# Kernel tuning notes

Measured on AMD Instinct MI355X. Metric: run time of the kernel, lower is better.

Reference implementation:

```python
import jax, jax.numpy as jnp
import numpy as np

DIM = 1024
HEADS = 16
HEAD_DIM = DIM // HEADS
MLP_HIDDEN = int(DIM * 0.7)  # 716
EPS = 1e-5


def _ln(x, g, b):
    m = jnp.mean(x, axis=-1, keepdims=True)
    v = jnp.mean(jnp.square(x - m), axis=-1, keepdims=True)
    return (x - m) * jax.lax.rsqrt(v + EPS) * g + b


def setup_inputs() -> dict:
    key = jax.random.key(0)
    ks = jax.random.split(key, 8)
    B, N = 4, 1024
    x = jax.random.normal(ks[0], (B, N, DIM), dtype=jnp.float32)
    s = 0.02
    return {
        "x": x,
        "norm_g": jnp.ones((DIM,), jnp.float32),
        "norm_b": jnp.zeros((DIM,), jnp.float32),
        "W1": jax.random.normal(ks[1], (DIM, 3 * DIM + MLP_HIDDEN), jnp.float32) * s,
        "b1": jnp.zeros((3 * DIM + MLP_HIDDEN,), jnp.float32),
        "qn_g": jnp.ones((HEAD_DIM,), jnp.float32),
        "qn_b": jnp.zeros((HEAD_DIM,), jnp.float32),
        "kn_g": jnp.ones((HEAD_DIM,), jnp.float32),
        "kn_b": jnp.zeros((HEAD_DIM,), jnp.float32),
        "projW": jax.random.normal(ks[2], (DIM, DIM), jnp.float32) * s,
        "projb": jnp.zeros((DIM,), jnp.float32),
        "mlpW": jax.random.normal(ks[3], (MLP_HIDDEN, DIM), jnp.float32) * s,  # mlp_bias=False
        "W2": jax.random.normal(ks[4], (2 * DIM, DIM), jnp.float32) * s,
        "b2": jnp.zeros((DIM,), jnp.float32),
        "ls_g": jnp.full((DIM,), 1e-5, jnp.float32),
    }


def reference(x, norm_g, norm_b, W1, b1, qn_g, qn_b, kn_g, kn_b,
              projW, projb, mlpW, W2, b2, ls_g):
    B, N, C = x.shape
    norm_x = _ln(x, norm_g, norm_b)
    f1 = norm_x @ W1 + b1  # (B, N, 3*dim + mlp_hidden)
    qkv, mlp_hidden = f1[..., :3 * DIM], f1[..., 3 * DIM:]
    # (B, N, 3, H, hd) -> (3, B, H, N, hd)
    qkv = qkv.reshape(B, N, 3, HEADS, HEAD_DIM).transpose(2, 0, 3, 1, 4)
    q, k, v = qkv[0], qkv[1], qkv[2]
    q = _ln(q, qn_g, qn_b)
    k = _ln(k, kn_g, kn_b)
    attn = jnp.einsum('bhnd,bhmd->bhnm', q, k) * (HEAD_DIM ** -0.5)
    attn = jax.nn.softmax(attn, axis=-1)
    xo = jnp.einsum('bhnm,bhmd->bhnd', attn, v)
    xo = xo.transpose(0, 2, 1, 3).reshape(B, N, DIM)
    attn_out = xo @ projW + projb
    mlp_out = jax.nn.gelu(mlp_hidden, approximate=False) @ mlpW  # no bias
    combined = jnp.concatenate([attn_out, mlp_out], axis=-1)
    out = x + (combined @ W2 + b2) * ls_g
    return out
```

## Files before the change

### kernel.cpp

```cpp
#include <hip/hip_runtime.h>
#include <cstdint>
#include <cstddef>

typedef unsigned short u16;
typedef unsigned char u8;
typedef __attribute__((ext_vector_type(8))) u16 u16x8;
typedef __attribute__((ext_vector_type(8))) __bf16 bf16x8;
typedef __attribute__((ext_vector_type(4))) float f32x4;
typedef __attribute__((ext_vector_type(16))) float f32x16;
typedef __attribute__((ext_vector_type(4))) int i32x4;
typedef __attribute__((ext_vector_type(8))) int i32x8;
typedef __attribute__((ext_vector_type(2))) int i32x2;

__device__ __forceinline__ u16 f2bf(float f) {
  unsigned u = __builtin_bit_cast(unsigned, f);
  return (u16)((u + 0x7FFFu + ((u >> 16) & 1u)) >> 16);
}
__device__ __forceinline__ float bf2f(u16 h) {
  return __builtin_bit_cast(float, (unsigned)h << 16);
}
__device__ __forceinline__ u8 f2fp8(float f) {
  return (u8)(__builtin_amdgcn_cvt_pk_fp8_f32(f, 0.f, 0, false) & 0xFF);
}
__device__ __forceinline__ f32x16 mfma32(u16x8 a, u16x8 b, f32x16 c) {
  return __builtin_amdgcn_mfma_f32_32x32x16_bf16(
      __builtin_bit_cast(bf16x8, a), __builtin_bit_cast(bf16x8, b), c, 0, 0, 0);
}
__device__ __forceinline__ unsigned cvtpk_bf16(float lo, float hi) {
  unsigned r;
  asm("v_cvt_pk_bf16_f32 %0, %1, %2" : "=v"(r) : "v"(lo), "v"(hi));
  return r;
}
__device__ __forceinline__ float exp2_fast(float x) {
  float r;
  asm("v_exp_f32 %0, %1" : "=v"(r) : "v"(x));
  return r;
}
__device__ __forceinline__ void plswap(unsigned& a, unsigned& b) {
  i32x2 r = __builtin_amdgcn_permlane32_swap((int)a, (int)b, false, false);
  a = (unsigned)r[0];
  b = (unsigned)r[1];
}
__device__ __forceinline__ void load_lds16(const void* g, void* l) {
  __builtin_amdgcn_global_load_lds(
      (const __attribute__((address_space(1))) void*)g,
      (__attribute__((address_space(3))) void*)l, 16, 0, 0);
}

__global__ __launch_bounds__(256) void k_pre(
    const float* __restrict__ W1, const float* __restrict__ projW,
    const float* __restrict__ mlpW, const float* __restrict__ W2,
    u8* __restrict__ W1t, u8* __restrict__ pWt, u8* __restrict__ mWt,
    u8* __restrict__ W2t, const float* __restrict__ x,
    const float* __restrict__ g, const float* __restrict__ b,
    u8* __restrict__ nx8) {
  __shared__ float t[32][33];
  __shared__ float red[8];
  const int L = blockIdx.x;
  const int tid = threadIdx.x;
  if (L < 7680) {
    const float* src;
    u8* dst;
    int R, C, dR, dC, bx, by;
    if (L < 3840) {
      src = W1; dst = W1t; R = 1024; C = 3788; dR = 1024; dC = 3840;
      bx = L % 120; by = L / 120;
    } else if (L < 4864) {
      int tq = L - 3840;
      src = projW; dst = pWt; R = 1024; C = 1024; dR = 1024; dC = 1024;
      bx = tq & 31; by = tq >> 5;
    } else if (L < 5632) {
      int tq = L - 4864;
      src = mlpW; dst = mWt; R = 716; C = 1024; dR = 768; dC = 1024;
      bx = tq & 31; by = tq >> 5;
    } else {
      int tq = L - 5632;
      src = W2; dst = W2t; R = 2048; C = 1024; dR = 2048; dC = 1024;
      bx = tq & 31; by = tq >> 5;
    }
    const int n0 = bx * 32, k0 = by * 32;
    const int tx = tid & 31, ty = tid >> 5;
#pragma unroll
    for (int j = 0; j < 4; ++j) {
      int kk = k0 + ty + 8 * j, nn = n0 + tx;
      float v = (kk < R && nn < C) ? src[(size_t)kk * C + nn] : 0.f;
      t[ty + 8 * j][tx] = v;
    }
    __syncthreads();
#pragma unroll
    for (int j = 0; j < 4; ++j) {
      int nn = n0 + ty + 8 * j, kk = k0 + tx;
      if (nn < dC && kk < dR) dst[(size_t)nn * dR + kk] = f2fp8(t[tx][ty + 8 * j]);
    }
  } else {
    const int row = L - 7680;
    float4 v = ((const float4*)(x + (size_t)row * 1024))[tid];
    float s = v.x + v.y + v.z + v.w;
    float ss = v.x * v.x + v.y * v.y + v.z * v.z + v.w * v.w;
#pragma unroll
    for (int off = 1; off < 64; off <<= 1) {
      s += __shfl_xor(s, off);
      ss += __shfl_xor(ss, off);
    }
    const int wid = tid >> 6, lane = tid & 63;
    if (lane == 0) { red[wid] = s; red[4 + wid] = ss; }
    __syncthreads();
    s = red[0] + red[1] + red[2] + red[3];
    ss = red[4] + red[5] + red[6] + red[7];
    const float mean = s * (1.f / 1024.f);
    const float var = ss * (1.f / 1024.f) - mean * mean;
    const float rstd = rsqrtf(var + 1e-5f);
    float4 gv = ((const float4*)g)[tid];
    float4 bv = ((const float4*)b)[tid];
    float y0 = (v.x - mean) * rstd * gv.x + bv.x;
    float y1 = (v.y - mean) * rstd * gv.y + bv.y;
    float y2 = (v.z - mean) * rstd * gv.z + bv.z;
    float y3 = (v.w - mean) * rstd * gv.w + bv.w;
    int pk = __builtin_amdgcn_cvt_pk_fp8_f32(y0, y1, 0, false);
    pk = __builtin_amdgcn_cvt_pk_fp8_f32(y2, y3, pk, true);
    ((int*)(nx8 + (size_t)row * 1024))[tid] = pk;
  }
}

__device__ __forceinline__ void gemm_fp8_core(const u8* __restrict__ A,
                                              const u8* __restrict__ B, int K,
                                              u8* Alds, u8* Blds,
                                              f32x16 (&acc)[2][2], int tid) {
  const int lane = tid & 63, wave = tid >> 6;
  const int h = lane >> 5, r32 = lane & 31;
  const int wrow = (wave >> 1) * 64, wcol = (wave & 1) * 64;
  const int srow0 = tid >> 2, spos = tid & 3;
  const int nk = K >> 6;
  auto STAGE = [&](int t, int bb) {
#pragma unroll
    for (int p = 0; p < 2; ++p) {
      const int row = p * 64 + srow0;
      const int c = spos ^ ((row >> 1) & 3);
      const size_t go = (size_t)row * K + (size_t)t * 64 + c * 16;
      load_lds16(A + go, Alds + bb * 8192 + (p * 256 + tid) * 16);
      load_lds16(B + go, Blds + bb * 8192 + (p * 256 + tid) * 16);
    }
  };
  STAGE(0, 0);
  STAGE(1, 1);
  asm volatile("s_waitcnt vmcnt(4)" ::: "memory");
  __builtin_amdgcn_s_barrier();
  int cur = 0;
  for (int kt = 0; kt < nk; ++kt) {
    const u8* Ac = Alds + cur * 8192;
    const u8* Bc = Blds + cur * 8192;
    i32x8 af[2], bf[2];
#pragma unroll
    for (int t = 0; t < 2; ++t) {
      {
        const int row = wrow + t * 32 + r32;
        const int sw = (row >> 1) & 3;
        i32x4 lo = *(const i32x4*)(Ac + row * 64 + ((2 * h) ^ sw) * 16);
        i32x4 hi = *(const i32x4*)(Ac + row * 64 + ((2 * h + 1) ^ sw) * 16);
        i32x8 a;
        a[0] = lo[0]; a[1] = lo[1]; a[2] = lo[2]; a[3] = lo[3];
        a[4] = hi[0]; a[5] = hi[1]; a[6] = hi[2]; a[7] = hi[3];
        af[t] = a;
      }
      {
        const int row = wcol + t * 32 + r32;
        const int sw = (row >> 1) & 3;
        i32x4 lo = *(const i32x4*)(Bc + row * 64 + ((2 * h) ^ sw) * 16);
        i32x4 hi = *(const i32x4*)(Bc + row * 64 + ((2 * h + 1) ^ sw) * 16);
        i32x8 b8;
        b8[0] = lo[0]; b8[1] = lo[1]; b8[2] = lo[2]; b8[3] = lo[3];
        b8[4] = hi[0]; b8[5] = hi[1]; b8[6] = hi[2]; b8[7] = hi[3];
        bf[t] = b8;
      }
    }
    if (kt + 2 < nk) STAGE(kt + 2, cur == 0 ? 2 : cur - 1);
#pragma unroll
    for (int i = 0; i < 2; ++i)
#pragma unroll
      for (int j = 0; j < 2; ++j)
        acc[i][j] = __builtin_amdgcn_mfma_scale_f32_32x32x64_f8f6f4(
            af[i], bf[j], acc[i][j], 0, 0, 0, 0x7F7F7F7F, 0, 0x7F7F7F7F);
    if (kt + 1 < nk) {
      if (kt + 2 < nk)
        asm volatile("s_waitcnt vmcnt(4)" ::: "memory");
      else
        asm volatile("s_waitcnt vmcnt(0)" ::: "memory");
      __builtin_amdgcn_s_barrier();
    }
    cur = (cur == 2) ? 0 : cur + 1;
  }
}

__device__ __forceinline__ void gemm_fp8_core64(const u8* __restrict__ A,
                                                const u8* __restrict__ B, int K,
                                                u8* Alds, u8* Blds,
                                                f32x16 (&acc)[2], int tid) {
  const int lane = tid & 63, wave = tid >> 6;
  const int h = lane >> 5, r32 = lane & 31;
  const int wrow = (wave >> 1) * 32, wcol = (wave & 1) * 64;
  const int nk = K >> 6;
  const int ra = tid >> 2, posa = tid & 3;
  const int ca = posa ^ ((ra >> 1) & 3);
  auto STAGE = [&](int t, int bb) {
    const size_t k0 = (size_t)t * 64;
    load_lds16(A + (size_t)ra * K + k0 + ca * 16, Alds + bb * 4096 + tid * 16);
#pragma unroll
    for (int p = 0; p < 2; ++p) {
      const int s = tid + 256 * p;
      const int r = s >> 2, pos = s & 3;
      const int c = pos ^ ((r >> 1) & 3);
      load_lds16(B + (size_t)r * K + k0 + c * 16, Blds + bb * 8192 + s * 16);
    }
  };
  STAGE(0, 0);
  STAGE(1, 1);
  asm volatile("s_waitcnt vmcnt(3)" ::: "memory");
  __builtin_amdgcn_s_barrier();
  int cur = 0;
  for (int kt = 0; kt < nk; ++kt) {
    const u8* Ac = Alds + cur * 4096;
    const u8* Bc = Blds + cur * 8192;
    i32x8 af, bf[2];
    {
      const int row = wrow + r32;
      const int sw = (row >> 1) & 3;
      i32x4 lo = *(const i32x4*)(Ac + row * 64 + ((2 * h) ^ sw) * 16);
      i32x4 hi = *(const i32x4*)(Ac + row * 64 + ((2 * h + 1) ^ sw) * 16);
      af[0] = lo[0]; af[1] = lo[1]; af[2] = lo[2]; af[3] = lo[3];
      af[4] = hi[0]; af[5] = hi[1]; af[6] = hi[2]; af[7] = hi[3];
    }
#pragma unroll
    for (int t = 0; t < 2; ++t) {
      const int row = wcol + t * 32 + r32;
      const int sw = (row >> 1) & 3;
      i32x4 lo = *(const i32x4*)(Bc + row * 64 + ((2 * h) ^ sw) * 16);
      i32x4 hi = *(const i32x4*)(Bc + row * 64 + ((2 * h + 1) ^ sw) * 16);
      i32x8 b8;
      b8[0] = lo[0]; b8[1] = lo[1]; b8[2] = lo[2]; b8[3] = lo[3];
      b8[4] = hi[0]; b8[5] = hi[1]; b8[6] = hi[2]; b8[7] = hi[3];
      bf[t] = b8;
    }
    if (kt + 2 < nk) STAGE(kt + 2, cur == 0 ? 2 : cur - 1);
#pragma unroll
    for (int j = 0; j < 2; ++j)
      acc[j] = __builtin_amdgcn_mfma_scale_f32_32x32x64_f8f6f4(
          af, bf[j], acc[j], 0, 0, 0, 0x7F7F7F7F, 0, 0x7F7F7F7F);
    if (kt + 1 < nk) {
      if (kt + 2 < nk)
        asm volatile("s_waitcnt vmcnt(3)" ::: "memory");
      else
        asm volatile("s_waitcnt vmcnt(0)" ::: "memory");
      __builtin_amdgcn_s_barrier();
    }
    cur = (cur == 2) ? 0 : cur + 1;
  }
}

__global__ __launch_bounds__(256) void k_gemm1(const u8* __restrict__ nx8,
                                               const u8* __restrict__ W1t,
                                               u16* __restrict__ f1,
                                               const float* __restrict__ b1) {
  __shared__ __align__(16) u8 Alds[3 * 128 * 64];
  __shared__ __align__(16) u8 Blds[3 * 128 * 64];
  const int tid = threadIdx.x, bm = blockIdx.y, bn = blockIdx.x;
  f32x16 acc[2][2];
#pragma unroll
  for (int i = 0; i < 2; ++i)
#pragma unroll
    for (int j = 0; j < 2; ++j)
#pragma unroll
      for (int r = 0; r < 16; ++r) acc[i][j][r] = 0.f;
  gemm_fp8_core(nx8 + (size_t)bm * 128 * 1024, W1t + (size_t)bn * 128 * 1024, 1024,
                Alds, Blds, acc, tid);
  const int lane = tid & 63, wave = tid >> 6;
  const int h = lane >> 5, r32 = lane & 31;
  const int wrow = (wave >> 1) * 64, wcol = (wave & 1) * 64;
#pragma unroll
  for (int i = 0; i < 2; ++i)
#pragma unroll
    for (int j = 0; j < 2; ++j) {
      const int col = bn * 128 + wcol + j * 32 + r32;
      const float bs = (col < 3788) ? b1[col] : 0.f;
#pragma unroll
      for (int r = 0; r < 16; ++r) {
        const int row = bm * 128 + wrow + i * 32 + 4 * h + (r & 3) + 8 * (r >> 2);
        f1[(size_t)row * 3840 + col] = f2bf(acc[i][j][r] + bs);
      }
    }
}

__global__ __launch_bounds__(256) void k_gemm_pm(
    const u8* __restrict__ xo, const u8* __restrict__ pWt,
    const u8* __restrict__ gel, const u8* __restrict__ mWt,
    u8* __restrict__ comb, const float* __restrict__ projb) {
  __shared__ __align__(16) u8 Alds[3 * 64 * 64];
  __shared__ __align__(16) u8 Blds[3 * 128 * 64];
  const int tid = threadIdx.x, bm = blockIdx.y, bnq = blockIdx.x;
  const u8* A;
  const u8* B;
  int K, colbase;
  const float* bias;
  if (bnq < 8) {
    A = xo + (size_t)bm * 64 * 1024;
    B = pWt + (size_t)bnq * 128 * 1024;
    K = 1024; colbase = bnq * 128; bias = projb;
  } else {
    A = gel + (size_t)bm * 64 * 768;
    B = mWt + (size_t)(bnq - 8) * 128 * 768;
    K = 768; colbase = 1024 + (bnq - 8) * 128; bias = nullptr;
  }
  f32x16 acc[2];
#pragma unroll
  for (int j = 0; j < 2; ++j)
#pragma unroll
    for (int r = 0; r < 16; ++r) acc[j][r] = 0.f;
  gemm_fp8_core64(A, B, K, Alds, Blds, acc, tid);
  const int lane = tid & 63, wave = tid >> 6;
  const int h = lane >> 5, r32 = lane & 31;
  const int wrow = (wave >> 1) * 32, wcol = (wave & 1) * 64;
#pragma unroll
  for (int j = 0; j < 2; ++j) {
    const int col = colbase + wcol + j * 32 + r32;
    const float bs = (bias != nullptr) ? bias[col] : 0.f;
#pragma unroll
    for (int r = 0; r < 16; ++r) {
      const int row = bm * 64 + wrow + 4 * h + (r & 3) + 8 * (r >> 2);
      comb[(size_t)row * 2048 + col] = f2fp8(acc[j][r] + bs);
    }
  }
}

__global__ __launch_bounds__(256) void k_gemm_fin(const u8* __restrict__ comb,
                                                  const u8* __restrict__ W2t,
                                                  float* __restrict__ out,
                                                  const float* __restrict__ b2,
                                                  const float* __restrict__ x,
                                                  const float* __restrict__ lsg) {
  __shared__ __align__(16) u8 Alds[3 * 64 * 64];
  __shared__ __align__(16) u8 Blds[3 * 128 * 64];
  const int tid = threadIdx.x, bm = blockIdx.y, bn = blockIdx.x;
  f32x16 acc[2];
#pragma unroll
  for (int j = 0; j < 2; ++j)
#pragma unroll
    for (int r = 0; r < 16; ++r) acc[j][r] = 0.f;
  gemm_fp8_core64(comb + (size_t)bm * 64 * 2048, W2t + (size_t)bn * 128 * 2048, 2048,
                  Alds, Blds, acc, tid);
  const int lane = tid & 63, wave = tid >> 6;
  const int h = lane >> 5, r32 = lane & 31;
  const int wrow = (wave >> 1) * 32, wcol = (wave & 1) * 64;
#pragma unroll
  for (int j = 0; j < 2; ++j) {
    const int col = bn * 128 + wcol + j * 32 + r32;
    const float bs = b2[col], ls = lsg[col];
#pragma unroll
    for (int r = 0; r < 16; ++r) {
      const int row = bm * 64 + wrow + 4 * h + (r & 3) + 8 * (r >> 2);
      out[(size_t)row * 1024 + col] =
          x[(size_t)row * 1024 + col] + (acc[j][r] + bs) * ls;
    }
  }
}

__global__ __launch_bounds__(256) void k_mid(const u16* __restrict__ f1,
                                             const float* __restrict__ qg,
                                             const float* __restrict__ qbb,
                                             const float* __restrict__ kg,
                                             const float* __restrict__ kbb,
                                             u16* __restrict__ q,
                                             u16* __restrict__ k,
                                             u8* __restrict__ gel,
                                             u16* __restrict__ vtb) {
  __shared__ u16 tt[32][33];
  const int tid = threadIdx.x;
  const int L = blockIdx.x;
  if (L < 4096) {
    const int row = L;
    const int rem = tid >> 3;
    const int which = rem >> 4, h = rem & 15;
    const int e8 = (tid & 7) * 8;
    u16x8 xv = *(const u16x8*)(f1 + (size_t)row * 3840 + which * 1024 + h * 64 + e8);
    float xf[8];
    float s1 = 0.f, s2 = 0.f;
#pragma unroll
    for (int e = 0; e < 8; ++e) {
      xf[e] = bf2f(xv[e]);
      s1 += xf[e];
      s2 += xf[e] * xf[e];
    }
#pragma unroll
    for (int off = 1; off < 8; off <<= 1) {
      s1 += __shfl_xor(s1, off);
      s2 += __shfl_xor(s2, off);
    }
    const float mean = s1 * (1.f / 64.f);
    const float var = s2 * (1.f / 64.f) - mean * mean;
    const float rstd = rsqrtf(var + 1e-5f);
    const float* g = (which == 0) ? qg : kg;
    const float* bb = (which == 0) ? qbb : kbb;
    float4 g0 = ((const float4*)g)[e8 >> 2], g1 = ((const float4*)g)[(e8 >> 2) + 1];
    float4 b0 = ((const float4*)bb)[e8 >> 2], b1 = ((const float4*)bb)[(e8 >> 2) + 1];
    float gv[8] = {g0.x, g0.y, g0.z, g0.w, g1.x, g1.y, g1.z, g1.w};
    float bv[8] = {b0.x, b0.y, b0.z, b0.w, b1.x, b1.y, b1.z, b1.w};
    u16x8 o;
#pragma unroll
    for (int e = 0; e < 8; ++e) o[e] = f2bf((xf[e] - mean) * rstd * gv[e] + bv[e]);
    const int b = row >> 10, n = row & 1023;
    u16* dst = (which == 0) ? q : k;
    *(u16x8*)(dst + ((size_t)(b * 16 + h) * 1024 + n) * 64 + e8) = o;
  } else if (L < 5632) {
    const int id = (L - 4096) * 256 + tid;
    const int row = id / 96, c8 = id - row * 96;
    u16x8 xv = *(const u16x8*)(f1 + (size_t)row * 3840 + 3072 + c8 * 8);
    float rr[8];
#pragma unroll
    for (int e = 0; e < 8; ++e) {
      const int col = c8 * 8 + e;
      rr[e] = 0.f;
      if (col < 716) {
        float xx = bf2f(xv[e]);
        rr[e] = 0.5f * xx * (1.f + erff(xx * 0.70710678118654752f));
      }
    }
    int p0 = __builtin_amdgcn_cvt_pk_fp8_f32(rr[0], rr[1], 0, false);
    p0 = __builtin_amdgcn_cvt_pk_fp8_f32(rr[2], rr[3], p0, true);
    int p1 = __builtin_amdgcn_cvt_pk_fp8_f32(rr[4], rr[5], 0, false);
    p1 = __builtin_amdgcn_cvt_pk_fp8_f32(rr[6], rr[7], p1, true);
    uint2 pk;
    pk.x = (unsigned)p0;
    pk.y = (unsigned)p1;
    *(uint2*)(gel + (size_t)row * 768 + c8 * 8) = pk;
  } else {
    const int t = L - 5632;
    const int xq = t & 1, yq = (t >> 1) & 31, z = t >> 6;
    const int b = z >> 4, h = z & 15;
    const int d0 = xq * 32, n0 = yq * 32;
    const int tx = tid & 31, ty = tid >> 5;
#pragma unroll
    for (int j = 0; j < 4; ++j)
      tt[ty + 8 * j][tx] =
          f1[(size_t)(b * 1024 + n0 + ty + 8 * j) * 3840 + 2048 + h * 64 + d0 + tx];
    __syncthreads();
#pragma unroll
    for (int j = 0; j < 4; ++j)
      vtb[(size_t)z * 65536 + (size_t)(d0 + ty + 8 * j) * 1024 + n0 + tx] =
          tt[tx][ty + 8 * j];
  }
}

__global__ __launch_bounds__(64) void k_flash(const u16* __restrict__ q,
                                              const u16* __restrict__ k,
                                              const u16* __restrict__ vt,
                                              u8* __restrict__ xo) {
  __shared__ __align__(16) u16 Kl[2][32 * 64];
  __shared__ __align__(16) u16 Vl[2][64 * 32];
  const int lane = threadIdx.x & 63;
  const int l31 = lane & 31, h = lane >> 5;
  const int L = blockIdx.x;
  const int xcd = L & 7, i = L >> 3;
  const int bh = xcd * 8 + (i & 7);
  const int qt = i >> 3;
  const int qrow0 = qt * 32;
  const u16* qb = q + ((size_t)bh * 1024 + qrow0) * 64;
  const u16* kb = k + (size_t)bh * 1024 * 64;
  const u16* vb = vt + (size_t)bh * 64 * 1024;

  u16x8 qf[4];
#pragma unroll
  for (int ds = 0; ds < 4; ++ds)
    qf[ds] = *(const u16x8*)(qb + (size_t)l31 * 64 + ds * 16 + h * 8);
  asm volatile("s_waitcnt vmcnt(0)" ::: "memory");

  f32x16 O[2];
#pragma unroll
  for (int d2 = 0; d2 < 2; ++d2)
#pragma unroll
    for (int r = 0; r < 16; ++r) O[d2][r] = 0.f;
  float lacc = 0.f;

  auto STAGE = [&](int t, int bb) {
#pragma unroll
    for (int p = 0; p < 4; ++p) {
      const int s = lane + 64 * p;
      const int kr = s >> 3, kslot = s & 7;
      const int kc = kslot ^ ((kr ^ (kr >> 3)) & 7);
      load_lds16(kb + (size_t)(t * 32 + kr) * 64 + kc * 8, (u16*)Kl[bb] + s * 8);
      const int vr = s >> 2, vslot = s & 3;
      const int vc = vslot ^ ((vr >> 1) & 3);
      load_lds16(vb + (size_t)vr * 1024 + t * 32 + vc * 8, (u16*)Vl[bb] + s * 8);
    }
  };
  STAGE(0, 0);
  STAGE(1, 1);

  const int swzk = (l31 & 7) ^ ((l31 >> 3) & 3);
  for (int t = 0; t < 32; ++t) {
    if (t < 31)
      asm volatile("s_waitcnt vmcnt(8)" ::: "memory");
    else
      asm volatile("s_waitcnt vmcnt(0)" ::: "memory");
    const u16* Kc = (const u16*)Kl[t & 1];
    const u16* Vc = (const u16*)Vl[t & 1];
    u16x8 kf[4], vf[4];
#pragma unroll
    for (int ds = 0; ds < 4; ++ds) {
      const int pos = (ds * 2 + h) ^ swzk;
      kf[ds] = *(const u16x8*)(Kc + l31 * 64 + pos * 8);
    }
#pragma unroll
    for (int m = 0; m < 2; ++m)
#pragma unroll
      for (int d2 = 0; d2 < 2; ++d2) {
        const int vr = d2 * 32 + l31;
        const int pos = (m * 2 + h) ^ ((vr >> 1) & 3);
        vf[m * 2 + d2] = *(const u16x8*)(Vc + vr * 32 + pos * 8);
      }
    asm volatile("s_waitcnt lgkmcnt(0)" ::: "memory");
    if (t + 2 < 32) STAGE(t + 2, t & 1);

    f32x16 S;
#pragma unroll
    for (int r = 0; r < 16; ++r) S[r] = 0.f;
    __builtin_amdgcn_s_setprio(1);
#pragma unroll
    for (int ds = 0; ds < 4; ++ds) S = mfma32(kf[ds], qf[ds], S);
    __builtin_amdgcn_s_setprio(0);

#pragma unroll
    for (int r = 0; r < 16; ++r) {
      float pv = exp2_fast(S[r] * 0.18033688011112042f);
      S[r] = pv;
      lacc += pv;
    }

    __builtin_amdgcn_s_setprio(1);
#pragma unroll
    for (int m = 0; m < 2; ++m) {
      const int ro = m * 8;
      unsigned w0 = cvtpk_bf16(S[ro + 0], S[ro + 1]);
      unsigned w2 = cvtpk_bf16(S[ro + 4], S[ro + 5]);
      unsigned w1 = cvtpk_bf16(S[ro + 2], S[ro + 3]);
      unsigned w3 = cvtpk_bf16(S[ro + 6], S[ro + 7]);
      plswap(w0, w2);
      plswap(w1, w3);
      i32x4 aw;
      aw[0] = (int)w0; aw[1] = (int)w1; aw[2] = (int)w2; aw[3] = (int)w3;
      const u16x8 pa = __builtin_bit_cast(u16x8, aw);
#pragma unroll
      for (int d2 = 0; d2 < 2; ++d2) O[d2] = mfma32(pa, vf[m * 2 + d2], O[d2]);
    }
    __builtin_amdgcn_s_setprio(0);
  }

  lacc += __shfl_xor(lacc, 32);
  const float inv = 1.f / lacc;
  const int b = bh >> 4, hh = bh & 15;
#pragma unroll
  for (int r = 0; r < 16; ++r) {
    const int qr = (r & 3) + 8 * (r >> 2) + 4 * h;
    const float invr = __shfl(inv, qr);
    u8* orow = xo + (size_t)(b * 1024 + qrow0 + qr) * 1024 + hh * 64;
    orow[l31] = f2fp8(O[0][r] * invr);
    orow[32 + l31] = f2fp8(O[1][r] * invr);
  }
}

extern "C" void kernel_launch(void* const* d_in, const int* in_sizes, int n_in,
                              void* d_out, int out_size, void* d_ws, size_t ws_size,
                              hipStream_t stream) {
  (void)in_sizes; (void)n_in; (void)out_size; (void)ws_size;
  const float* x      = (const float*)d_in[0];
  const float* norm_g = (const float*)d_in[1];
  const float* norm_b = (const float*)d_in[2];
  const float* W1     = (const float*)d_in[3];
  const float* b1     = (const float*)d_in[4];
  const float* qn_g   = (const float*)d_in[5];
  const float* qn_b   = (const float*)d_in[6];
  const float* kn_g   = (const float*)d_in[7];
  const float* kn_b   = (const float*)d_in[8];
  const float* projW  = (const float*)d_in[9];
  const float* projb  = (const float*)d_in[10];
  const float* mlpW   = (const float*)d_in[11];
  const float* W2     = (const float*)d_in[12];
  const float* b2     = (const float*)d_in[13];
  const float* ls_g   = (const float*)d_in[14];

  char* ws = (char*)d_ws;
  u8*  W1t8 = (u8*)(ws + 0);
  u8*  pWt8 = (u8*)(ws + 3932160);
  u8*  mWt8 = (u8*)(ws + 4980736);
  u8*  W2t8 = (u8*)(ws + 5767168);
  u8*  nx8  = (u8*)(ws + 7864320);
  u16* f1   = (u16*)(ws + 12058624);
  u16* qbuf = (u16*)(ws + 43515904);
  u16* kbuf = (u16*)(ws + 51904512);
  u16* vtb  = (u16*)(ws + 60293120);
  u8*  gel8 = (u8*)(ws + 68681728);

  k_pre<<<11776, 256, 0, stream>>>(W1, projW, mlpW, W2, W1t8, pWt8, mWt8, W2t8,
                                   x, norm_g, norm_b, nx8);
  k_gemm1<<<dim3(30, 32), 256, 0, stream>>>(nx8, W1t8, f1, b1);
  k_mid<<<9728, 256, 0, stream>>>(f1, qn_g, qn_b, kn_g, kn_b, qbuf, kbuf, gel8,
                                  vtb);
  k_flash<<<2048, 64, 0, stream>>>(qbuf, kbuf, vtb, nx8);
  k_gemm_pm<<<dim3(16, 64), 256, 0, stream>>>(nx8, pWt8, gel8, mWt8, (u8*)f1, projb);
  k_gemm_fin<<<dim3(8, 64), 256, 0, stream>>>((u8*)f1, W2t8, (float*)d_out, b2, x,
                                              ls_g);
}
```

Measured before the change: 234.0 us.

## Fuse q/k LayerNorm and GELU into GEMM1 epilogue; software-pipeline flash QK

The GEMM1 epilogue now applies the per-head q/k LayerNorm and writes directly into the head-major q/k buffers, and applies exact GELU and fp8 quantization for the MLP-hidden columns. This removes the bf16 round trip through f1 for those columns, and k_mid shrinks to only the V transpose. The flash kernel is also software-pipelined: the next tile's QK^T MFMAs are issued before the current tile's softmax/PV work, using double-buffered S and V fragments. In exchange, register pressure rises in both kernels, the epilogue does strided scalar stores plus shuffle reductions, and erf now runs inside the GEMM.

```diff
diff --git a/kernel.cpp b/kernel.cpp
--- a/kernel.cpp
+++ b/kernel.cpp
@@ -256,10 +256,12 @@
   }
 }
 
-__global__ __launch_bounds__(256) void k_gemm1(const u8* __restrict__ nx8,
-                                               const u8* __restrict__ W1t,
-                                               u16* __restrict__ f1,
-                                               const float* __restrict__ b1) {
+__global__ __launch_bounds__(256) void k_gemm1(
+    const u8* __restrict__ nx8, const u8* __restrict__ W1t, u16* __restrict__ f1,
+    const float* __restrict__ b1, const float* __restrict__ qg,
+    const float* __restrict__ qb_, const float* __restrict__ kg,
+    const float* __restrict__ kb_, u16* __restrict__ qbuf, u16* __restrict__ kbuf,
+    u8* __restrict__ gel8) {
   __shared__ __align__(16) u8 Alds[3 * 128 * 64];
   __shared__ __align__(16) u8 Blds[3 * 128 * 64];
   const int tid = threadIdx.x, bm = blockIdx.y, bn = blockIdx.x;
@@ -275,18 +277,68 @@
   const int lane = tid & 63, wave = tid >> 6;
   const int h = lane >> 5, r32 = lane & 31;
   const int wrow = (wave >> 1) * 64, wcol = (wave & 1) * 64;
-#pragma unroll
-  for (int i = 0; i < 2; ++i)
-#pragma unroll
-    for (int j = 0; j < 2; ++j) {
-      const int col = bn * 128 + wcol + j * 32 + r32;
-      const float bs = (col < 3788) ? b1[col] : 0.f;
+  if (bn < 16) {
+    const int wc = bn * 128 + wcol;
+    const int which = wc >> 10;
+    const int head = (wc >> 6) & 15;
+    const float* g = which ? kg : qg;
+    const float* bb = which ? kb_ : qb_;
+    const float g0 = g[r32], g1 = g[32 + r32];
+    const float be0 = bb[r32], be1 = bb[32 + r32];
+    const float bias0 = b1[wc + r32], bias1 = b1[wc + 32 + r32];
+    u16* dst = which ? kbuf : qbuf;
+#pragma unroll
+    for (int i = 0; i < 2; ++i)
 #pragma unroll
       for (int r = 0; r < 16; ++r) {
+        float v0 = acc[i][0][r] + bias0;
+        float v1 = acc[i][1][r] + bias1;
+        float s = v0 + v1, ss = v0 * v0 + v1 * v1;
+#pragma unroll
+        for (int off = 1; off < 32; off <<= 1) {
+          s += __shfl_xor(s, off);
+          ss += __shfl_xor(ss, off);
+        }
+        const float mean = s * (1.f / 64.f);
+        const float var = ss * (1.f / 64.f) - mean * mean;
+        const float rstd = rsqrtf(var + 1e-5f);
         const int row = bm * 128 + wrow + i * 32 + 4 * h + (r & 3) + 8 * (r >> 2);
-        f1[(size_t)row * 3840 + col] = f2bf(acc[i][j][r] + bs);
+        const int b = row >> 10, n = row & 1023;
+        u16* orow = dst + ((size_t)(b * 16 + head) * 1024 + n) * 64;
+        orow[r32] = f2bf((v0 - mean) * rstd * g0 + be0);
+        orow[32 + r32] = f2bf((v1 - mean) * rstd * g1 + be1);
       }
-    }
+  } else if (bn < 24) {
+#pragma unroll
+    for (int i = 0; i < 2; ++i)
+#pragma unroll
+      for (int j = 0; j < 2; ++j) {
+        const int col = bn * 128 + wcol + j * 32 + r32;
+        const float bs = b1[col];
+#pragma unroll
+        for (int r = 0; r < 16; ++r) {
+          const int row = bm * 128 + wrow + i * 32 + 4 * h + (r & 3) + 8 * (r >> 2);
+          f1[(size_t)row * 3840 + col] = f2bf(acc[i][j][r] + bs);
+        }
+      }
+  } else {
+#pragma unroll
+    for (int i = 0; i < 2; ++i)
+#pragma unroll
+      for (int j = 0; j < 2; ++j) {
+        const int col = bn * 128 + wcol + j * 32 + r32;
+        const int c = col - 3072;
+        const bool ok = (col < 3788);
+        const float bs = ok ? b1[col] : 0.f;
+#pragma unroll
+        for (int r = 0; r < 16; ++r) {
+          const int row = bm * 128 + wrow + i * 32 + 4 * h + (r & 3) + 8 * (r >> 2);
+          float y = acc[i][j][r] + bs;
+          float ge = ok ? 0.5f * y * (1.f + erff(y * 0.70710678118654752f)) : 0.f;
+          gel8[(size_t)row * 768 + c] = f2fp8(ge);
+        }
+      }
+  }
 }
 
 __global__ __launch_bounds__(256) void k_gemm_pm(
@@ -363,89 +415,23 @@
 }
 
 __global__ __launch_bounds__(256) void k_mid(const u16* __restrict__ f1,
-                                             const float* __restrict__ qg,
-                                             const float* __restrict__ qbb,
-                                             const float* __restrict__ kg,
-                                             const float* __restrict__ kbb,
-                                             u16* __restrict__ q,
-                                             u16* __restrict__ k,
-                                             u8* __restrict__ gel,
                                              u16* __restrict__ vtb) {
   __shared__ u16 tt[32][33];
   const int tid = threadIdx.x;
-  const int L = blockIdx.x;
-  if (L < 4096) {
-    const int row = L;
-    const int rem = tid >> 3;
-    const int which = rem >> 4, h = rem & 15;
-    const int e8 = (tid & 7) * 8;
-    u16x8 xv = *(const u16x8*)(f1 + (size_t)row * 3840 + which * 1024 + h * 64 + e8);
-    float xf[8];
-    float s1 = 0.f, s2 = 0.f;
-#pragma unroll
-    for (int e = 0; e < 8; ++e) {
-      xf[e] = bf2f(xv[e]);
-      s1 += xf[e];
-      s2 += xf[e] * xf[e];
-    }
-#pragma unroll
-    for (int off = 1; off < 8; off <<= 1) {
-      s1 += __shfl_xor(s1, off);
-      s2 += __shfl_xor(s2, off);
-    }
-    const float mean = s1 * (1.f / 64.f);
-    const float var = s2 * (1.f / 64.f) - mean * mean;
-    const float rstd = rsqrtf(var + 1e-5f);
-    const float* g = (which == 0) ? qg : kg;
-    const float* bb = (which == 0) ? qbb : kbb;
-    float4 g0 = ((const float4*)g)[e8 >> 2], g1 = ((const float4*)g)[(e8 >> 2) + 1];
-    float4 b0 = ((const float4*)bb)[e8 >> 2], b1 = ((const float4*)bb)[(e8 >> 2) + 1];
-    float gv[8] = {g0.x, g0.y, g0.z, g0.w, g1.x, g1.y, g1.z, g1.w};
-    float bv[8] = {b0.x, b0.y, b0.z, b0.w, b1.x, b1.y, b1.z, b1.w};
-    u16x8 o;
-#pragma unroll
-    for (int e = 0; e < 8; ++e) o[e] = f2bf((xf[e] - mean) * rstd * gv[e] + bv[e]);
-    const int b = row >> 10, n = row & 1023;
-    u16* dst = (which == 0) ? q : k;
-    *(u16x8*)(dst + ((size_t)(b * 16 + h) * 1024 + n) * 64 + e8) = o;
-  } else if (L < 5632) {
-    const int id = (L - 4096) * 256 + tid;
-    const int row = id / 96, c8 = id - row * 96;
-    u16x8 xv = *(const u16x8*)(f1 + (size_t)row * 3840 + 3072 + c8 * 8);
-    float rr[8];
-#pragma unroll
-    for (int e = 0; e < 8; ++e) {
-      const int col = c8 * 8 + e;
-      rr[e] = 0.f;
-      if (col < 716) {
-        float xx = bf2f(xv[e]);
-        rr[e] = 0.5f * xx * (1.f + erff(xx * 0.70710678118654752f));
-      }
-    }
-    int p0 = __builtin_amdgcn_cvt_pk_fp8_f32(rr[0], rr[1], 0, false);
-    p0 = __builtin_amdgcn_cvt_pk_fp8_f32(rr[2], rr[3], p0, true);
-    int p1 = __builtin_amdgcn_cvt_pk_fp8_f32(rr[4], rr[5], 0, false);
-    p1 = __builtin_amdgcn_cvt_pk_fp8_f32(rr[6], rr[7], p1, true);
-    uint2 pk;
-    pk.x = (unsigned)p0;
-    pk.y = (unsigned)p1;
-    *(uint2*)(gel + (size_t)row * 768 + c8 * 8) = pk;
-  } else {
-    const int t = L - 5632;
-    const int xq = t & 1, yq = (t >> 1) & 31, z = t >> 6;
-    const int b = z >> 4, h = z & 15;
-    const int d0 = xq * 32, n0 = yq * 32;
-    const int tx = tid & 31, ty = tid >> 5;
-#pragma unroll
-    for (int j = 0; j < 4; ++j)
-      tt[ty + 8 * j][tx] =
-          f1[(size_t)(b * 1024 + n0 + ty + 8 * j) * 3840 + 2048 + h * 64 + d0 + tx];
-    __syncthreads();
-#pragma unroll
-    for (int j = 0; j < 4; ++j)
-      vtb[(size_t)z * 65536 + (size_t)(d0 + ty + 8 * j) * 1024 + n0 + tx] =
-          tt[tx][ty + 8 * j];
-  }
+  const int t = blockIdx.x;
+  const int xq = t & 1, yq = (t >> 1) & 31, z = t >> 6;
+  const int b = z >> 4, h = z & 15;
+  const int d0 = xq * 32, n0 = yq * 32;
+  const int tx = tid & 31, ty = tid >> 5;
+#pragma unroll
+  for (int j = 0; j < 4; ++j)
+    tt[ty + 8 * j][tx] =
+        f1[(size_t)(b * 1024 + n0 + ty + 8 * j) * 3840 + 2048 + h * 64 + d0 + tx];
+  __syncthreads();
+#pragma unroll
+  for (int j = 0; j < 4; ++j)
+    vtb[(size_t)z * 65536 + (size_t)(d0 + ty + 8 * j) * 1024 + n0 + tx] =
+        tt[tx][ty + 8 * j];
 }
 
 __global__ __launch_bounds__(64) void k_flash(const u16* __restrict__ q,
@@ -494,19 +480,17 @@
   STAGE(1, 1);
 
   const int swzk = (l31 & 7) ^ ((l31 >> 3) & 3);
-  for (int t = 0; t < 32; ++t) {
-    if (t < 31)
-      asm volatile("s_waitcnt vmcnt(8)" ::: "memory");
-    else
-      asm volatile("s_waitcnt vmcnt(0)" ::: "memory");
+  const float C = 0.18033688011112042f;
+
+  f32x16 Sa, Sb;
+  u16x8 vfA[4], vfB[4];
+
+  auto READ_FRAGS = [&](int t, u16x8 (&kf)[4], u16x8 (&vf)[4]) {
     const u16* Kc = (const u16*)Kl[t & 1];
     const u16* Vc = (const u16*)Vl[t & 1];
-    u16x8 kf[4], vf[4];
-#pragma unroll
-    for (int ds = 0; ds < 4; ++ds) {
-      const int pos = (ds * 2 + h) ^ swzk;
-      kf[ds] = *(const u16x8*)(Kc + l31 * 64 + pos * 8);
-    }
+#pragma unroll
+    for (int ds = 0; ds < 4; ++ds)
+      kf[ds] = *(const u16x8*)(Kc + l31 * 64 + (((ds * 2 + h) ^ swzk)) * 8);
 #pragma unroll
     for (int m = 0; m < 2; ++m)
 #pragma unroll
@@ -515,41 +499,69 @@
         const int pos = (m * 2 + h) ^ ((vr >> 1) & 3);
         vf[m * 2 + d2] = *(const u16x8*)(Vc + vr * 32 + pos * 8);
       }
+  };
+
+  {
+    asm volatile("s_waitcnt vmcnt(8)" ::: "memory");
+    u16x8 kf[4];
+    READ_FRAGS(0, kf, vfA);
     asm volatile("s_waitcnt lgkmcnt(0)" ::: "memory");
-    if (t + 2 < 32) STAGE(t + 2, t & 1);
-
-    f32x16 S;
-#pragma unroll
-    for (int r = 0; r < 16; ++r) S[r] = 0.f;
+    __builtin_amdgcn_sched_barrier(0);
+    STAGE(2, 0);
+#pragma unroll
+    for (int r = 0; r < 16; ++r) Sa[r] = 0.f;
     __builtin_amdgcn_s_setprio(1);
 #pragma unroll
-    for (int ds = 0; ds < 4; ++ds) S = mfma32(kf[ds], qf[ds], S);
+    for (int ds = 0; ds < 4; ++ds) Sa = mfma32(kf[ds], qf[ds], Sa);
     __builtin_amdgcn_s_setprio(0);
-
+  }
+
+  auto TILE = [&](int t, f32x16& Sc, f32x16& Sn, u16x8 (&vc)[4], u16x8 (&vn)[4]) {
+    if (t < 31) {
+      if (t <= 29)
+        asm volatile("s_waitcnt vmcnt(8)" ::: "memory");
+      else
+        asm volatile("s_waitcnt vmcnt(0)" ::: "memory");
+      u16x8 kf[4];
+      READ_FRAGS(t + 1, kf, vn);
+      asm volatile("s_waitcnt lgkmcnt(0)" ::: "memory");
+      __builtin_amdgcn_sched_barrier(0);
+      if (t + 3 < 32) STAGE(t + 3, (t + 3) & 1);
+#pragma unroll
+      for (int r = 0; r < 16; ++r) Sn[r] = 0.f;
+      __builtin_amdgcn_s_setprio(1);
+#pragma unroll
+      for (int ds = 0; ds < 4; ++ds) Sn = mfma32(kf[ds], qf[ds], Sn);
+      __builtin_amdgcn_s_setprio(0);
+    }
 #pragma unroll
     for (int r = 0; r < 16; ++r) {
-      float pv = exp2_fast(S[r] * 0.18033688011112042f);
-      S[r] = pv;
+      float pv = exp2_fast(Sc[r] * C);
+      Sc[r] = pv;
       lacc += pv;
     }
-
     __builtin_amdgcn_s_setprio(1);
 #pragma unroll
     for (int m = 0; m < 2; ++m) {
       const int ro = m * 8;
-      unsigned w0 = cvtpk_bf16(S[ro + 0], S[ro + 1]);
-      unsigned w2 = cvtpk_bf16(S[ro + 4], S[ro + 5]);
-      unsigned w1 = cvtpk_bf16(S[ro + 2], S[ro + 3]);
-      unsigned w3 = cvtpk_bf16(S[ro + 6], S[ro + 7]);
+      unsigned w0 = cvtpk_bf16(Sc[ro + 0], Sc[ro + 1]);
+      unsigned w2 = cvtpk_bf16(Sc[ro + 4], Sc[ro + 5]);
+      unsigned w1 = cvtpk_bf16(Sc[ro + 2], Sc[ro + 3]);
+      unsigned w3 = cvtpk_bf16(Sc[ro + 6], Sc[ro + 7]);
       plswap(w0, w2);
       plswap(w1, w3);
       i32x4 aw;
       aw[0] = (int)w0; aw[1] = (int)w1; aw[2] = (int)w2; aw[3] = (int)w3;
       const u16x8 pa = __builtin_bit_cast(u16x8, aw);
 #pragma unroll
-      for (int d2 = 0; d2 < 2; ++d2) O[d2] = mfma32(pa, vf[m * 2 + d2], O[d2]);
+      for (int d2 = 0; d2 < 2; ++d2) O[d2] = mfma32(pa, vc[m * 2 + d2], O[d2]);
     }
     __builtin_amdgcn_s_setprio(0);
+  };
+
+  for (int t = 0; t < 32; t += 2) {
+    TILE(t, Sa, Sb, vfA, vfB);
+    TILE(t + 1, Sb, Sa, vfB, vfA);
   }
 
   lacc += __shfl_xor(lacc, 32);
@@ -599,9 +611,9 @@
 
   k_pre<<<11776, 256, 0, stream>>>(W1, projW, mlpW, W2, W1t8, pWt8, mWt8, W2t8,
                                    x, norm_g, norm_b, nx8);
-  k_gemm1<<<dim3(30, 32), 256, 0, stream>>>(nx8, W1t8, f1, b1);
-  k_mid<<<9728, 256, 0, stream>>>(f1, qn_g, qn_b, kn_g, kn_b, qbuf, kbuf, gel8,
-                                  vtb);
+  k_gemm1<<<dim3(30, 32), 256, 0, stream>>>(nx8, W1t8, f1, b1, qn_g, qn_b, kn_g,
+                                            kn_b, qbuf, kbuf, gel8);
+  k_mid<<<4096, 256, 0, stream>>>(f1, vtb);
   k_flash<<<2048, 64, 0, stream>>>(qbuf, kbuf, vtb, nx8);
   k_gemm_pm<<<dim3(16, 64), 256, 0, stream>>>(nx8, pWt8, gel8, mWt8, (u8*)f1, projb);
   k_gemm_fin<<<dim3(8, 64), 256, 0, stream>>>((u8*)f1, W2t8, (float*)d_out, b2, x,
```

Result: no change. 231.8 us (-0.9%).
